# Performance work log

Measured on AMD Instinct MI355X. Metric: run time of the kernel, lower is better.

## Reference

```python
import jax, jax.numpy as jnp
import numpy as np

N_NODES = 100000


def setup_inputs() -> dict:
    key = jax.random.key(0)
    k1, k2, k3, k4, k5 = jax.random.split(key, 5)
    K, N, Z, F = 2, N_NODES, 128, 128
    E = 1600000
    x = jax.random.normal(k1, (K, N, Z), dtype=jnp.float32)
    adj_rows = jax.random.randint(k2, (E,), 0, N, dtype=jnp.int32)
    adj_cols = jax.random.randint(k3, (E,), 0, N, dtype=jnp.int32)
    adj_vals = jax.random.uniform(k4, (E,), dtype=jnp.float32)
    # xavier_uniform_ for [Z, F]
    limit = float(np.sqrt(6.0 / (Z + F)))
    weight = jax.random.uniform(k5, (Z, F), dtype=jnp.float32, minval=-limit, maxval=limit)
    return {"x": x, "adj_rows": adj_rows, "adj_cols": adj_cols,
            "adj_vals": adj_vals, "weight": weight}


def reference(x, adj_rows, adj_cols, adj_vals, weight):
    # dropout p=0.0 -> identity
    # support[k] = x[k] @ W  (shared weight across the K MIMO channels)
    support = jnp.einsum('knz,zf->knf', x, weight)  # [K, N, F]

    def spmm(sup):  # sparse adj (COO) @ dense [N, F]
        gathered = adj_vals[:, None] * sup[adj_cols]          # [E, F]
        return jax.ops.segment_sum(gathered, adj_rows, num_segments=N_NODES)

    # K is small and fixed; loop to avoid materializing [K, E, F] at once
    out = jnp.stack([spmm(support[k]) for k in range(support.shape[0])], axis=0)
    return jax.nn.relu(out)
```

## Files before the change

### kernel.cpp

```cpp
#include <hip/hip_runtime.h>

#define KCH 2
#define ZF 128
#define CHUNK 256
#define BSH 9
typedef unsigned short u16;

using bf16x8_t = __attribute__((ext_vector_type(8))) short;
using f32x4_t  = __attribute__((ext_vector_type(4))) float;
using f32x4n   = __attribute__((ext_vector_type(4))) float;

__device__ inline u16 f2bf(float f) {
  unsigned u = __float_as_uint(f);
  return (u16)((u + 0x7FFF + ((u >> 16) & 1)) >> 16);
}
__device__ inline float bf2f(u16 h) { return __uint_as_float((unsigned)h << 16); }

__global__ __launch_bounds__(256) void zero_and_wfrag(
    int* __restrict__ p, int n, int nbN,
    const float* __restrict__ W, u16* __restrict__ wf) {
  if ((int)blockIdx.x < nbN) {
    int i = blockIdx.x * 256 + threadIdx.x;
    if (i < n) p[i] = 0;
    return;
  }
  int t = (blockIdx.x - nbN) * 256 + threadIdx.x;
  if (t >= 16384) return;
  int k = t >> 7, f = t & 127;
  int ks = k >> 5, kk = k & 31;
  int lg = kk >> 3, j = kk & 7;
  int ft = f >> 4, c = f & 15;
  int l = lg * 16 + c;
  int e = ((ft * 4 + ks) * 64 + l) * 8 + j;
  float w = W[t];
  u16 hi = f2bf(w);
  u16 lo = f2bf(w - bf2f(hi));
  wf[e] = hi;
  wf[16384 + e] = lo;
}


__global__ __launch_bounds__(256) void coarse_hist(
    const int* __restrict__ rows, int* __restrict__ gcnt,
    int E, int chunk, int NB) {
  __shared__ int lc[256];
  int t = threadIdx.x;
  lc[t] = 0;
  __syncthreads();
  int b0 = blockIdx.x * chunk;
  int b1 = min(E, b0 + chunk);
  for (int i = b0 + t; i < b1; i += 256)
    atomicAdd(&lc[rows[i] >> BSH], 1);
  __syncthreads();
  if (t < NB && lc[t]) atomicAdd(&gcnt[t], lc[t]);
}

__global__ __launch_bounds__(256) void bucket_scan(
    int* __restrict__ cw, int NB, int E, int* __restrict__ row_off, int N) {
  __shared__ int s[256];
  int t = threadIdx.x;
  int v = (t < NB) ? cw[t] : 0;
  s[t] = v;
  __syncthreads();
#pragma unroll
  for (int o = 1; o < 256; o <<= 1) {
    int u = (t >= o) ? s[t - o] : 0;
    __syncthreads();
    s[t] += u;
    __syncthreads();
  }
  int ex = s[t] - v;
  if (t < NB) { cw[256 + t] = ex; cw[512 + t] = ex; }
  if (t == 0) { cw[512 + NB] = E; row_off[N] = E; }
}

__global__ __launch_bounds__(256) void coarse_scatter(
    const int* __restrict__ rows, const int* __restrict__ cols,
    const float* __restrict__ vals, int* __restrict__ gcursor,
    int2* __restrict__ binned_rc, float* __restrict__ binned_v,
    int E, int chunk, int NB) {
  __shared__ int lc[256];
  __shared__ int lcur[256];
  int t = threadIdx.x;
  lc[t] = 0;
  __syncthreads();
  int b0 = blockIdx.x * chunk;
  int b1 = min(E, b0 + chunk);
  for (int i = b0 + t; i < b1; i += 256)
    atomicAdd(&lc[rows[i] >> BSH], 1);
  __syncthreads();
  if (t < NB) lcur[t] = lc[t] ? atomicAdd(&gcursor[t], lc[t]) : 0;
  __syncthreads();
  for (int i = b0 + t; i < b1; i += 256) {
    int r = rows[i];
    int p = atomicAdd(&lcur[r >> BSH], 1);
    binned_rc[p] = make_int2(r, cols[i]);
    binned_v[p] = vals[i];
  }
}

__global__ __launch_bounds__(256) void fine_sort(
    const int2* __restrict__ binned_rc, const float* __restrict__ binned_v,
    const int* __restrict__ bbase, int2* __restrict__ pairs,
    int* __restrict__ row_off, int N) {
  int b = blockIdx.x;
  int beg = bbase[b];
  int endb = bbase[b + 1];
  int row0 = b << BSH;
  int nr = min(1 << BSH, N - row0);
  __shared__ int cnt[512];
  __shared__ int s2[256];
  __shared__ int cur[512];
  int t = threadIdx.x;
  cnt[t] = 0;
  cnt[t + 256] = 0;
  __syncthreads();
  for (int i = beg + t; i < endb; i += 256)
    atomicAdd(&cnt[binned_rc[i].x - row0], 1);
  __syncthreads();
  int c0 = cnt[2 * t], c1 = cnt[2 * t + 1];
  s2[t] = c0 + c1;
  __syncthreads();
#pragma unroll
  for (int o = 1; o < 256; o <<= 1) {
    int u = (t >= o) ? s2[t - o] : 0;
    __syncthreads();
    s2[t] += u;
    __syncthreads();
  }
  int exb = s2[t] - (c0 + c1);
  cur[2 * t] = beg + exb;
  cur[2 * t + 1] = beg + exb + c0;
  if (2 * t < nr)     row_off[row0 + 2 * t]     = beg + exb;
  if (2 * t + 1 < nr) row_off[row0 + 2 * t + 1] = beg + exb + c0;
  __syncthreads();
  for (int i = beg + t; i < endb; i += 256) {
    int2 rc = binned_rc[i];
    float v = binned_v[i];
    int p = atomicAdd(&cur[rc.x - row0], 1);
    pairs[p] = make_int2(rc.y, __float_as_int(v));
  }
}

__global__ __launch_bounds__(256) void hist_kernel(
    const int* __restrict__ rows, int* __restrict__ cnt, int E) {
  int i = blockIdx.x * 256 + threadIdx.x;
  if (i < E) atomicAdd(&cnt[rows[i]], 1);
}

__global__ __launch_bounds__(256) void chunk_reduce(
    const int* __restrict__ cnt, int* __restrict__ chunk, int N) {
  __shared__ int s[256];
  int tid = threadIdx.x;
  int i = blockIdx.x * 256 + tid;
  s[tid] = (i < N) ? cnt[i] : 0;
  __syncthreads();
#pragma unroll
  for (int o = 128; o > 0; o >>= 1) {
    if (tid < o) s[tid] += s[tid + o];
    __syncthreads();
  }
  if (tid == 0) chunk[blockIdx.x] = s[0];
}

__global__ __launch_bounds__(512) void chunk_scan(
    int* __restrict__ chunk, int nch, int* __restrict__ row_off, int N, int E) {
  __shared__ int s[512];
  int tid = threadIdx.x;
  int v = (tid < nch) ? chunk[tid] : 0;
  s[tid] = v;
  __syncthreads();
#pragma unroll
  for (int o = 1; o < 512; o <<= 1) {
    int t = (tid >= o) ? s[tid - o] : 0;
    __syncthreads();
    s[tid] += t;
    __syncthreads();
  }
  if (tid < nch) chunk[tid] = s[tid] - v;
  if (tid == 0) row_off[N] = E;
}

__global__ __launch_bounds__(256) void scan_within_chunk(
    const int* __restrict__ cnt, const int* __restrict__ chunk,
    int* __restrict__ row_off, int* __restrict__ cursor, int N) {
  __shared__ int s[256];
  int tid = threadIdx.x;
  int i = blockIdx.x * 256 + tid;
  int v = (i < N) ? cnt[i] : 0;
  s[tid] = v;
  __syncthreads();
#pragma unroll
  for (int o = 1; o < 256; o <<= 1) {
    int t = (tid >= o) ? s[tid - o] : 0;
    __syncthreads();
    s[tid] += t;
    __syncthreads();
  }
  if (i < N) {
    int start = chunk[blockIdx.x] + s[tid] - v;
    row_off[i] = start;
    cursor[i] = start;
  }
}

__global__ __launch_bounds__(256) void bucket_kernel(
    const int* __restrict__ rows, const int* __restrict__ cols,
    const float* __restrict__ vals, int* __restrict__ cursor,
    int2* __restrict__ pairs, int E) {
  int i = blockIdx.x * 256 + threadIdx.x;
  if (i >= E) return;
  int r = rows[i];
  int p = atomicAdd(&cursor[r], 1);
  int2 pr;
  pr.x = cols[i];
  pr.y = __float_as_int(vals[i]);
  pairs[p] = pr;
}

__global__ __launch_bounds__(256) void gemm_xw_bf16(
    const float* __restrict__ x, const u16* __restrict__ wf,
    u16* __restrict__ xi, int N) {
  __shared__ u16 lw[32768];
  int tid = threadIdx.x;
  {
    const uint4* src = (const uint4*)wf;
    uint4* dst = (uint4*)lw;
#pragma unroll
    for (int i = 0; i < 16; ++i) dst[tid + i * 256] = src[tid + i * 256];
  }
  __syncthreads();

  int l   = tid & 63;
  int col = l & 15;
  int rg  = l >> 4;
  int wgid = blockIdx.x * 4 + (tid >> 6);
  int nt = (KCH * N) >> 4;
  int nw = gridDim.x * 4;

  for (int t = wgid; t < nt; t += nw) {
    int row0 = t << 4;
    int kc = (row0 >= N) ? 1 : 0;
    int n0 = row0 - kc * N;

    const float* xb = x + (size_t)(kc * N + n0 + col) * ZF + rg * 8;
    bf16x8_t bhi[4], blo[4];
#pragma unroll
    for (int ks = 0; ks < 4; ++ks) {
      f32x4n u = __builtin_nontemporal_load((const f32x4n*)(xb + ks * 32));
      f32x4n v = __builtin_nontemporal_load(((const f32x4n*)(xb + ks * 32)) + 1);
      float tmp[8] = {u[0], u[1], u[2], u[3], v[0], v[1], v[2], v[3]};
#pragma unroll
      for (int j = 0; j < 8; ++j) {
        u16 hi = f2bf(tmp[j]);
        bhi[ks][j] = (short)hi;
        blo[ks][j] = (short)f2bf(tmp[j] - bf2f(hi));
      }
    }

    f32x4_t acc[8];
#pragma unroll
    for (int ft = 0; ft < 8; ++ft) acc[ft] = {0.f, 0.f, 0.f, 0.f};

#pragma unroll
    for (int ft = 0; ft < 8; ++ft) {
#pragma unroll
      for (int ks = 0; ks < 4; ++ks) {
        int eb = ((ft * 4 + ks) * 64 + l) * 8;
        const bf16x8_t ahi = *(const bf16x8_t*)(lw + eb);
        const bf16x8_t alo = *(const bf16x8_t*)(lw + 16384 + eb);
        acc[ft] = __builtin_amdgcn_mfma_f32_16x16x32_bf16(ahi, bhi[ks], acc[ft], 0, 0, 0);
        acc[ft] = __builtin_amdgcn_mfma_f32_16x16x32_bf16(alo, bhi[ks], acc[ft], 0, 0, 0);
        acc[ft] = __builtin_amdgcn_mfma_f32_16x16x32_bf16(ahi, blo[ks], acc[ft], 0, 0, 0);
      }
    }

    u16* dst = xi + (size_t)(n0 + col) * 256 + kc * 128;
#pragma unroll
    for (int ft = 0; ft < 8; ++ft) {
      ushort4 o;
      o.x = f2bf(acc[ft][0]);
      o.y = f2bf(acc[ft][1]);
      o.z = f2bf(acc[ft][2]);
      o.w = f2bf(acc[ft][3]);
      *(ushort4*)(dst + ft * 16 + rg * 4) = o;
    }
  }
}

__global__ __launch_bounds__(256) void spmm_csr_bf16(
    const u16* __restrict__ xi, const int* __restrict__ row_off,
    const int2* __restrict__ pairs, float* __restrict__ out, int N,
    int r0, int rcnt) {
  int rr = blockIdx.x * 4 + (threadIdx.x >> 6);
  if (rr >= rcnt) return;
  int r = r0 + rr;
  if (r >= N) return;
  int lane = threadIdx.x & 63;
  int beg = row_off[r];
  int end = row_off[r + 1];

  float4 acc = make_float4(0.f, 0.f, 0.f, 0.f);
  int j = beg;
  for (; j + 4 <= end; j += 4) {
    int2 p0 = pairs[j + 0];
    int2 p1 = pairs[j + 1];
    int2 p2 = pairs[j + 2];
    int2 p3 = pairs[j + 3];
    ushort4 a0 = ((const ushort4*)(xi + (size_t)p0.x * 256))[lane];
    ushort4 a1 = ((const ushort4*)(xi + (size_t)p1.x * 256))[lane];
    ushort4 a2 = ((const ushort4*)(xi + (size_t)p2.x * 256))[lane];
    ushort4 a3 = ((const ushort4*)(xi + (size_t)p3.x * 256))[lane];
    float v0 = __int_as_float(p0.y);
    float v1 = __int_as_float(p1.y);
    float v2 = __int_as_float(p2.y);
    float v3 = __int_as_float(p3.y);
    acc.x = fmaf(v0, bf2f(a0.x), acc.x);
    acc.y = fmaf(v0, bf2f(a0.y), acc.y);
    acc.z = fmaf(v0, bf2f(a0.z), acc.z);
    acc.w = fmaf(v0, bf2f(a0.w), acc.w);
    acc.x = fmaf(v1, bf2f(a1.x), acc.x);
    acc.y = fmaf(v1, bf2f(a1.y), acc.y);
    acc.z = fmaf(v1, bf2f(a1.z), acc.z);
    acc.w = fmaf(v1, bf2f(a1.w), acc.w);
    acc.x = fmaf(v2, bf2f(a2.x), acc.x);
    acc.y = fmaf(v2, bf2f(a2.y), acc.y);
    acc.z = fmaf(v2, bf2f(a2.z), acc.z);
    acc.w = fmaf(v2, bf2f(a2.w), acc.w);
    acc.x = fmaf(v3, bf2f(a3.x), acc.x);
    acc.y = fmaf(v3, bf2f(a3.y), acc.y);
    acc.z = fmaf(v3, bf2f(a3.z), acc.z);
    acc.w = fmaf(v3, bf2f(a3.w), acc.w);
  }
  for (; j < end; ++j) {
    int2 p = pairs[j];
    ushort4 a = ((const ushort4*)(xi + (size_t)p.x * 256))[lane];
    float v = __int_as_float(p.y);
    acc.x = fmaf(v, bf2f(a.x), acc.x);
    acc.y = fmaf(v, bf2f(a.y), acc.y);
    acc.z = fmaf(v, bf2f(a.z), acc.z);
    acc.w = fmaf(v, bf2f(a.w), acc.w);
  }
  f32x4n o;
  o[0] = fmaxf(acc.x, 0.f);
  o[1] = fmaxf(acc.y, 0.f);
  o[2] = fmaxf(acc.z, 0.f);
  o[3] = fmaxf(acc.w, 0.f);
  int k = lane >> 5;
  int g = lane & 31;
  __builtin_nontemporal_store(o, ((f32x4n*)(out + ((size_t)k * N + (size_t)r) * ZF)) + g);
}

__global__ __launch_bounds__(256) void spmm_csr(
    const float* __restrict__ x, const int* __restrict__ row_off,
    const int2* __restrict__ pairs, float* __restrict__ out, int N) {
  int r = blockIdx.x * 4 + (threadIdx.x >> 6);
  int lane = threadIdx.x & 63;
  if (r >= N) return;
  int k = lane >> 5;
  int g = lane & 31;
  int beg = row_off[r];
  int end = row_off[r + 1];
  const float* xb = x + (size_t)k * N * ZF;
  float4 acc = make_float4(0.f, 0.f, 0.f, 0.f);
  for (int j = beg; j < end; ++j) {
    int2 p = pairs[j];
    float4 a = ((const float4*)(xb + (size_t)p.x * ZF))[g];
    float v = __int_as_float(p.y);
    acc.x = fmaf(v, a.x, acc.x);
    acc.y = fmaf(v, a.y, acc.y);
    acc.z = fmaf(v, a.z, acc.z);
    acc.w = fmaf(v, a.w, acc.w);
  }
  ((float4*)(out + ((size_t)k * N + (size_t)r) * ZF))[g] = acc;
}

__device__ inline void atomic_add_f32(float* p, float v) {
#if defined(__HIP_DEVICE_COMPILE__) && defined(__AMDGCN__)
  unsafeAtomicAdd(p, v);
#else
  atomicAdd(p, v);
#endif
}

__global__ __launch_bounds__(256) void zero_kernel(float4* __restrict__ p, long long n4) {
  long long i = (long long)blockIdx.x * 256 + threadIdx.x;
  long long stride = (long long)gridDim.x * 256;
  for (; i < n4; i += stride) p[i] = make_float4(0.f, 0.f, 0.f, 0.f);
}

__global__ __launch_bounds__(256) void scatter_spmm_kernel(
    const float* __restrict__ x, const int* __restrict__ rows,
    const int* __restrict__ cols, const float* __restrict__ vals,
    float* __restrict__ tmp, int E, int N) {
  int t = blockIdx.x * 256 + threadIdx.x;
  int e = t >> 6;
  if (e >= E) return;
  int sub = t & 63;
  int k = sub >> 5;
  int g = sub & 31;
  int row = rows[e];
  int col = cols[e];
  float val = vals[e];
  const float4* src = (const float4*)(x + ((size_t)k * N + col) * ZF);
  float4 v = src[g];
  float* dst = tmp + ((size_t)k * N + row) * ZF + (size_t)g * 4;
  atomic_add_f32(dst + 0, val * v.x);
  atomic_add_f32(dst + 1, val * v.y);
  atomic_add_f32(dst + 2, val * v.z);
  atomic_add_f32(dst + 3, val * v.w);
}

__global__ __launch_bounds__(256) void gemm_relu_inplace(
    float* __restrict__ io, const float* __restrict__ W, long long Mtotal) {
  __shared__ float Ws[64 * ZF];
  __shared__ float Xs[32 * ZF];
  int tid = threadIdx.x;
  long long row0 = (long long)blockIdx.x * 32;

  const float4* src = (const float4*)(io + row0 * ZF);
  float4* Xs4 = (float4*)Xs;
#pragma unroll
  for (int i = 0; i < 4; ++i) {
    int idx = tid + i * 256;
    long long r = row0 + (idx >> 5);
    Xs4[idx] = (r < Mtotal) ? src[idx] : make_float4(0.f, 0.f, 0.f, 0.f);
  }

  int f0 = (tid & 31) * 4;
  int rg = tid >> 5;

  float acc[4][4];
#pragma unroll
  for (int j = 0; j < 4; ++j)
#pragma unroll
    for (int i = 0; i < 4; ++i) acc[j][i] = 0.f;

  const float4* W4 = (const float4*)W;
  float4* Ws4 = (float4*)Ws;

  for (int zh = 0; zh < 2; ++zh) {
    __syncthreads();
#pragma unroll
    for (int i = 0; i < 8; ++i) {
      int idx = tid + i * 256;
      Ws4[idx] = W4[(size_t)zh * 2048 + idx];
    }
    __syncthreads();

#pragma unroll 4
    for (int z = 0; z < 64; ++z) {
      float4 wv = *(const float4*)(Ws + z * ZF + f0);
#pragma unroll
      for (int j = 0; j < 4; ++j) {
        float xv = Xs[(rg + 8 * j) * ZF + (zh * 64 + z)];
        acc[j][0] = fmaf(xv, wv.x, acc[j][0]);
        acc[j][1] = fmaf(xv, wv.y, acc[j][1]);
        acc[j][2] = fmaf(xv, wv.z, acc[j][2]);
        acc[j][3] = fmaf(xv, wv.w, acc[j][3]);
      }
    }
  }

#pragma unroll
  for (int j = 0; j < 4; ++j) {
    long long r = row0 + rg + 8 * j;
    if (r < Mtotal) {
      float4 o;
      o.x = fmaxf(acc[j][0], 0.f);
      o.y = fmaxf(acc[j][1], 0.f);
      o.z = fmaxf(acc[j][2], 0.f);
      o.w = fmaxf(acc[j][3], 0.f);
      *(float4*)(io + r * ZF + f0) = o;
    }
  }
}

extern "C" void kernel_launch(void* const* d_in, const int* in_sizes, int n_in,
                              void* d_out, int out_size, void* d_ws, size_t ws_size,
                              hipStream_t stream) {
  const float* x    = (const float*)d_in[0];
  const int*   rows = (const int*)d_in[1];
  const int*   cols = (const int*)d_in[2];
  const float* vals = (const float*)d_in[3];
  const float* W    = (const float*)d_in[4];

  int E = in_sizes[1];
  int N = in_sizes[0] / (KCH * ZF);
  float* out = (float*)d_out;

  int nch = (N + CHUNK - 1) / CHUNK;

  size_t off = 0;
  auto carve = [&](size_t bytes) {
    size_t p = off;
    off += (bytes + 15) & ~(size_t)15;
    return (char*)d_ws + p;
  };
  int*  row_off = (int*)carve((size_t)(N + 1) * 4);
  int*  cursor  = (int*)carve((size_t)N * 4);
  int*  chunk   = (int*)carve((size_t)nch * 4);
  int2* pairs   = (int2*)carve((size_t)E * 8);
  size_t off_csr = off;
  u16*  wf      = (u16*)carve(65536);
  u16*  xi      = (u16*)carve((size_t)N * KCH * ZF * 2);

  bool csr_ok  = (off_csr <= ws_size) && (nch <= 512);
  bool bf16_ok = (off <= ws_size) && (nch <= 512) && ((N & 15) == 0);

  int NB = (N + (1 << BSH) - 1) >> BSH;
  bool binned_ok = bf16_ok && (NB <= 256) && (N >= 1024) &&
                   ((size_t)E * 12 <= (size_t)N * KCH * ZF * 2);

  if (csr_ok) {
    int nb_E = (E + 255) / 256;

    if (binned_ok) {
      int2*  binned_rc = (int2*)xi;
      float* binned_v  = (float*)((char*)xi + (size_t)E * 8);
      int*   cw        = cursor;
      int GA = 512;
      int chunkE = (E + GA - 1) / GA;

      zero_and_wfrag<<<1 + 64, 256, 0, stream>>>(cw, 256, 1, W, wf);
      coarse_hist<<<GA, 256, 0, stream>>>(rows, cw, E, chunkE, NB);
      bucket_scan<<<1, 256, 0, stream>>>(cw, NB, E, row_off, N);
      coarse_scatter<<<GA, 256, 0, stream>>>(rows, cols, vals, cw + 256,
                                             binned_rc, binned_v, E, chunkE, NB);
      fine_sort<<<NB, 256, 0, stream>>>(binned_rc, binned_v, cw + 512,
                                        pairs, row_off, N);
      gemm_xw_bf16<<<512, 256, 0, stream>>>(x, wf, xi, N);
      int sblocks = (N + 3) / 4;
      spmm_csr_bf16<<<sblocks, 256, 0, stream>>>(xi, row_off, pairs, out, N, 0, N);
    } else {
      int nb_N = (N + 255) / 256;
      int wblocks = bf16_ok ? 64 : 0;
      zero_and_wfrag<<<nb_N + wblocks, 256, 0, stream>>>(cursor, N, nb_N, W, wf);
      hist_kernel<<<nb_E, 256, 0, stream>>>(rows, cursor, E);
      chunk_reduce<<<nch, 256, 0, stream>>>(cursor, chunk, N);
      chunk_scan<<<1, 512, 0, stream>>>(chunk, nch, row_off, N, E);
      scan_within_chunk<<<nch, 256, 0, stream>>>(cursor, chunk, row_off, cursor, N);
      bucket_kernel<<<nb_E, 256, 0, stream>>>(rows, cols, vals, cursor, pairs, E);

      int sblocks = (N + 3) / 4;
      if (bf16_ok) {
        gemm_xw_bf16<<<512, 256, 0, stream>>>(x, wf, xi, N);
        spmm_csr_bf16<<<sblocks, 256, 0, stream>>>(xi, row_off, pairs, out, N, 0, N);
      } else {
        spmm_csr<<<sblocks, 256, 0, stream>>>(x, row_off, pairs, out, N);
        long long Mtotal = (long long)KCH * N;
        int mblocks = (int)((Mtotal + 31) / 32);
        gemm_relu_inplace<<<mblocks, 256, 0, stream>>>(out, W, Mtotal);
      }
    }
  } else {
    long long n4 = (long long)out_size / 4;
    int zblocks = (int)((n4 + 255) / 256);
    zero_kernel<<<zblocks, 256, 0, stream>>>((float4*)out, n4);
    long long total_threads = (long long)E * 64;
    int sblocks = (int)((total_threads + 255) / 256);
    scatter_spmm_kernel<<<sblocks, 256, 0, stream>>>(x, rows, cols, vals, out, E, N);
    long long Mtotal = (long long)KCH * N;
    int mblocks = (int)((Mtotal + 31) / 32);
    gemm_relu_inplace<<<mblocks, 256, 0, stream>>>(out, W, Mtotal);
  }
}
```

Baseline: 468.0 us.

## Widen fine_sort to 512 threads, halve coarse blocks, split SpMM launches

fine_sort now runs 512 threads per bin, one row per thread, and does a 512-wide scan instead of a paired 256-wide scan. The coarse histogram and scatter grid drops from 512 to 256 blocks, so each block handles more edges. The SpMM launch is split into four sequential launches over row quarters, which adds launch overhead and may change cache locality. Together these retune how the preprocessing and SpMM work is spread across blocks, at the cost of a scan with more barrier steps and more kernel launches.

```diff
diff --git a/kernel.cpp b/kernel.cpp
--- a/kernel.cpp
+++ b/kernel.cpp
@@ -99,7 +99,7 @@
   }
 }
 
-__global__ __launch_bounds__(256) void fine_sort(
+__global__ __launch_bounds__(512) void fine_sort(
     const int2* __restrict__ binned_rc, const float* __restrict__ binned_v,
     const int* __restrict__ bbase, int2* __restrict__ pairs,
     int* __restrict__ row_off, int N) {
@@ -109,36 +109,33 @@
   int row0 = b << BSH;
   int nr = min(1 << BSH, N - row0);
   __shared__ int cnt[512];
-  __shared__ int s2[256];
+  __shared__ int s[512];
   __shared__ int cur[512];
   int t = threadIdx.x;
   cnt[t] = 0;
-  cnt[t + 256] = 0;
-  __syncthreads();
-  for (int i = beg + t; i < endb; i += 256)
+  __syncthreads();
+  for (int i = beg + t; i < endb; i += 512)
     atomicAdd(&cnt[binned_rc[i].x - row0], 1);
   __syncthreads();
-  int c0 = cnt[2 * t], c1 = cnt[2 * t + 1];
-  s2[t] = c0 + c1;
-  __syncthreads();
-#pragma unroll
-  for (int o = 1; o < 256; o <<= 1) {
-    int u = (t >= o) ? s2[t - o] : 0;
-    __syncthreads();
-    s2[t] += u;
-    __syncthreads();
-  }
-  int exb = s2[t] - (c0 + c1);
-  cur[2 * t] = beg + exb;
-  cur[2 * t + 1] = beg + exb + c0;
-  if (2 * t < nr)     row_off[row0 + 2 * t]     = beg + exb;
-  if (2 * t + 1 < nr) row_off[row0 + 2 * t + 1] = beg + exb + c0;
-  __syncthreads();
-  for (int i = beg + t; i < endb; i += 256) {
+  int v = cnt[t];
+  s[t] = v;
+  __syncthreads();
+#pragma unroll
+  for (int o = 1; o < 512; o <<= 1) {
+    int u = (t >= o) ? s[t - o] : 0;
+    __syncthreads();
+    s[t] += u;
+    __syncthreads();
+  }
+  int ex = s[t] - v;
+  cur[t] = beg + ex;
+  if (t < nr) row_off[row0 + t] = beg + ex;
+  __syncthreads();
+  for (int i = beg + t; i < endb; i += 512) {
     int2 rc = binned_rc[i];
-    float v = binned_v[i];
+    float vv = binned_v[i];
     int p = atomicAdd(&cur[rc.x - row0], 1);
-    pairs[p] = make_int2(rc.y, __float_as_int(v));
+    pairs[p] = make_int2(rc.y, __float_as_int(vv));
   }
 }
 
@@ -519,7 +516,7 @@
       int2*  binned_rc = (int2*)xi;
       float* binned_v  = (float*)((char*)xi + (size_t)E * 8);
       int*   cw        = cursor;
-      int GA = 512;
+      int GA = 256;
       int chunkE = (E + GA - 1) / GA;
 
       zero_and_wfrag<<<1 + 64, 256, 0, stream>>>(cw, 256, 1, W, wf);
@@ -527,11 +524,17 @@
       bucket_scan<<<1, 256, 0, stream>>>(cw, NB, E, row_off, N);
       coarse_scatter<<<GA, 256, 0, stream>>>(rows, cols, vals, cw + 256,
                                              binned_rc, binned_v, E, chunkE, NB);
-      fine_sort<<<NB, 256, 0, stream>>>(binned_rc, binned_v, cw + 512,
+      fine_sort<<<NB, 512, 0, stream>>>(binned_rc, binned_v, cw + 512,
                                         pairs, row_off, N);
       gemm_xw_bf16<<<512, 256, 0, stream>>>(x, wf, xi, N);
-      int sblocks = (N + 3) / 4;
-      spmm_csr_bf16<<<sblocks, 256, 0, stream>>>(xi, row_off, pairs, out, N, 0, N);
+      int q = (N + 3) / 4;
+      for (int i = 0; i < 4; ++i) {
+        int r0 = i * q;
+        int rcnt = (r0 + q <= N) ? q : (N - r0);
+        if (rcnt <= 0) break;
+        int blocks = (rcnt + 3) / 4;
+        spmm_csr_bf16<<<blocks, 256, 0, stream>>>(xi, row_off, pairs, out, N, r0, rcnt);
+      }
     } else {
       int nb_N = (N + 255) / 256;
       int wblocks = bf16_ok ? 64 : 0;
```

Result: no change. 469.5 us (+0.3%).
